# Optimization experiments

Hardware: AMD Instinct MI355X
Metric: run time of the kernel (lower is better)

The kernel has to match this reference:

```python
import jax, jax.numpy as jnp
import numpy as np
from itertools import product as iter_product

N_QUBITS = 6
DIM = 2 ** N_QUBITS            # 64
N_GEN = DIM * DIM - 1          # 4095
DEPTH = 4
N_OBS = 15

_GENS = None

def _build_generators(n):
    I = np.eye(2, dtype=np.complex64)
    X = np.array([[0, 1], [1, 0]], np.complex64)
    Y = np.array([[0, -1j], [1j, 0]], np.complex64)
    Z = np.array([[1, 0], [0, -1]], np.complex64)
    P = [I, X, Y, Z]
    gens = []
    for idx in iter_product(range(4), repeat=n):
        if all(i == 0 for i in idx):
            continue
        m = P[idx[0]]
        for k in range(1, n):
            m = np.kron(m, P[idx[k]])
        gens.append(m)
    return jnp.asarray(np.stack(gens))  # [4^n-1, 2^n, 2^n] complex64

def _gens():
    global _GENS
    if _GENS is None:
        _GENS = _build_generators(N_QUBITS)
    return _GENS

def _apply_ry(psi, q, theta, n):
    # psi: [B, 2^n] complex; RY(theta) on qubit q
    B = psi.shape[0]
    x = psi.reshape(B, 2 ** q, 2, 2 ** (n - q - 1))
    c = jnp.cos(theta / 2)
    s = jnp.sin(theta / 2)
    s0, s1 = x[:, :, 0, :], x[:, :, 1, :]
    x = jnp.stack([c * s0 - s * s1, s * s0 + c * s1], axis=2)
    return x.reshape(B, -1)

def _apply_cnot(psi, c, t, n):
    # psi: [B, 2^n]; CNOT control c, target t
    B = psi.shape[0]
    x = psi.reshape((B,) + (2,) * n)
    ax_c, ax_t = 1 + c, 1 + t
    x0 = jnp.take(x, 0, axis=ax_c)
    x1 = jnp.take(x, 1, axis=ax_c)
    ax_t2 = ax_t - (1 if ax_t > ax_c else 0)
    x1 = jnp.flip(x1, axis=ax_t2)
    x = jnp.stack([x0, x1], axis=ax_c)
    return x.reshape(B, -1)

def _make_hermitians(A, B, D):
    # create_Hermitian vectorized over the m observables.
    # h[i,j] = A[idx]+iB[idx] for j<i (row-major lower-tri), h[i-1,i-1]=D[i];
    # then H = h + h^H.
    il, jl = jnp.tril_indices(DIM, -1)  # row-major order matches count+j loop
    di = jnp.arange(DIM - 1)

    def one(a, b, d):
        h = jnp.zeros((DIM, DIM), jnp.complex64)
        h = h.at[il, jl].set(a + 1j * b)
        h = h.at[di, di].set(d[1:].astype(jnp.complex64))
        return h + h.conj().T

    return jax.vmap(one)(A, B, D)  # [m, DIM, DIM]

def setup_inputs() -> dict:
    key = jax.random.key(0)
    ks = jax.random.split(key, 8)
    batch, input_dim, hidden = 256, 1024, 2047
    n_off = DIM * (DIM - 1) // 2  # 2016
    return {
        "x": jax.random.normal(ks[0], (batch, input_dim), jnp.float32),
        "W1": 0.02 * jax.random.normal(ks[1], (input_dim, hidden), jnp.float32),
        "b1": jnp.zeros((hidden,), jnp.float32),
        "W2": 0.02 * jax.random.normal(ks[2], (hidden, N_GEN), jnp.float32),
        "b2": jnp.zeros((N_GEN,), jnp.float32),
        "var_params": 0.01 * jax.random.normal(ks[3], (DEPTH, N_QUBITS), jnp.float32),
        "A": 2.0 * jax.random.normal(ks[4], (N_OBS, n_off), jnp.float32),
        "B": 2.0 * jax.random.normal(ks[5], (N_OBS, n_off), jnp.float32),
        "D": 2.0 * jax.random.normal(ks[6], (N_OBS, DIM), jnp.float32),
    }

def reference(x, W1, b1, W2, b2, var_params, A, B, D):
    n = N_QUBITS
    # encoding projection: Linear -> SiLU -> Linear
    h = jax.nn.silu(x @ W1 + b1)
    theta = h @ W2 + b2  # [batch, 4^n - 1]
    gens = _gens()  # [n_gen, dim, dim] complex64 (constant)
    # A_mat = sum_g theta_g G_g (Hermitian), U = exp(i A_mat)
    Amat = jnp.einsum('bg,gij->bij', theta.astype(jnp.complex64), gens)
    U = jax.vmap(jax.scipy.linalg.expm)(1j * Amat)  # [batch, dim, dim]
    psi = U[:, :, 0]  # apply to |0...0>
    # hardware-efficient VQC: RY layer + CNOT ring per depth
    for d in range(DEPTH):
        for q in range(n):
            psi = _apply_ry(psi, q, var_params[d, q], n)
        for q in range(n):
            psi = _apply_cnot(psi, q, (q + 1) % n, n)
    H = _make_hermitians(A, B, D)  # [m, dim, dim]
    # expectation <psi|H_w|psi>
    exp = jnp.einsum('bi,wij,bj->bw', psi.conj(), H, psi).real
    return exp  # [batch, n_observables]
```

## Files before the change

kernel.cpp:

```cpp
#include <hip/hip_runtime.h>
#include <math.h>

typedef unsigned short ushort_t;
typedef __attribute__((ext_vector_type(8))) short bf16x8_t;
typedef __attribute__((ext_vector_type(4))) float f32x4_t;

__device__ __forceinline__ void tsplit(float v, unsigned& h, unsigned& l) {
  unsigned u = __float_as_uint(v);
  h = u >> 16;
  float lo = v - __uint_as_float(u & 0xffff0000u);
  l = __float_as_uint(lo) >> 16;
}

__device__ __forceinline__ void split8(const float* p, bf16x8_t& hi, bf16x8_t& lo) {
#pragma unroll
  for (int e = 0; e < 8; ++e) {
    unsigned h, l;
    tsplit(p[e], h, l);
    hi[e] = (short)h;
    lo[e] = (short)l;
  }
}

#define LSTR 40

__global__ __launch_bounds__(512) void gemm1_kernel(
    const float* __restrict__ x, const float* __restrict__ W1,
    const float* __restrict__ b1,
    ushort_t* __restrict__ hh, ushort_t* __restrict__ hl) {
  __shared__ __align__(16) ushort_t As[2][32 * LSTR];
  __shared__ __align__(16) ushort_t Bs[2][64 * LSTR];
  const int t = threadIdx.x;
  const int lane = t & 63;
  const int wv = t >> 6;
  const int l15 = lane & 15;
  const int quad = lane >> 4;
  const int wm = wv & 1;
  const int wn = wv >> 1;
  const int m0 = (blockIdx.x >> 5) * 32;
  const int n0 = (blockIdx.x & 31) * 64;

  f32x4_t acc = (f32x4_t){0.f, 0.f, 0.f, 0.f};

  const int xrow = (t & 127) >> 2;
  const int xkq  = (t & 3) * 8;
  const int wu   = t - 128;
  const int wnx  = wu & 63;
  const int wkh  = (wu >> 6) & 3;
  const bool wok = (n0 + wnx) < 2047;

  for (int k0 = 0; k0 < 1024; k0 += 32) {
    if (t < 128) {
      const float* src = x + (size_t)(m0 + xrow) * 1024 + k0 + xkq;
      float p[8];
      float4 va = *(const float4*)src;
      float4 vb = *(const float4*)(src + 4);
      p[0] = va.x; p[1] = va.y; p[2] = va.z; p[3] = va.w;
      p[4] = vb.x; p[5] = vb.y; p[6] = vb.z; p[7] = vb.w;
      bf16x8_t hi, lo;
      split8(p, hi, lo);
      *(bf16x8_t*)&As[0][xrow * LSTR + xkq] = hi;
      *(bf16x8_t*)&As[1][xrow * LSTR + xkq] = lo;
    } else if (t < 384) {
      float p[8];
#pragma unroll
      for (int i = 0; i < 8; ++i) {
        int k = k0 + wkh * 8 + i;
        p[i] = wok ? W1[(size_t)k * 2047 + n0 + wnx] : 0.f;
      }
      bf16x8_t hi, lo;
      split8(p, hi, lo);
      *(bf16x8_t*)&Bs[0][wnx * LSTR + wkh * 8] = hi;
      *(bf16x8_t*)&Bs[1][wnx * LSTR + wkh * 8] = lo;
    }
    __syncthreads();
    const int nr = wn * 16 + l15;
    bf16x8_t bfh = *(const bf16x8_t*)&Bs[0][nr * LSTR + quad * 8];
    bf16x8_t bfl = *(const bf16x8_t*)&Bs[1][nr * LSTR + quad * 8];
    const int mr = wm * 16 + l15;
    bf16x8_t afh = *(const bf16x8_t*)&As[0][mr * LSTR + quad * 8];
    bf16x8_t afl = *(const bf16x8_t*)&As[1][mr * LSTR + quad * 8];
    acc = __builtin_amdgcn_mfma_f32_16x16x32_bf16(afh, bfh, acc, 0, 0, 0);
    acc = __builtin_amdgcn_mfma_f32_16x16x32_bf16(afh, bfl, acc, 0, 0, 0);
    acc = __builtin_amdgcn_mfma_f32_16x16x32_bf16(afl, bfh, acc, 0, 0, 0);
    __syncthreads();
  }
  const int col = n0 + wn * 16 + l15;
#pragma unroll
  for (int rg = 0; rg < 4; ++rg) {
    int row = m0 + wm * 16 + quad * 4 + rg;
    float v = acc[rg];
    if (col < 2047) {
      v += b1[col];
      v = v / (1.f + expf(-v));
    } else {
      v = 0.f;
    }
    unsigned h, l;
    tsplit(v, h, l);
    size_t o = (size_t)row * 2048 + col;
    hh[o] = (ushort_t)h;
    hl[o] = (ushort_t)l;
  }
}

__global__ __launch_bounds__(256) void gemm2k_kernel(
    const ushort_t* __restrict__ Ah, const ushort_t* __restrict__ Al,
    const float* __restrict__ W2,
    float* __restrict__ part) {
  __shared__ __align__(16) ushort_t Ab[2][128 * LSTR];
  __shared__ __align__(16) ushort_t Bb[2][64 * LSTR];
  const int t = threadIdx.x;
  const int lane = t & 63;
  const int wv = t >> 6;
  const int l15 = lane & 15;
  const int quad = lane >> 4;
  const int wm = wv >> 1, wn = wv & 1;
  const int m0 = blockIdx.y * 128;
  const int n0 = blockIdx.x * 64;
  const int ks = blockIdx.z;

  const int wu  = t - 128;
  const int bn  = wu & 63;
  const int bkh = (wu >> 6) & 1;
  const bool bok = (n0 + bn) < 4095;

  f32x4_t acc[4][2];
#pragma unroll
  for (int i = 0; i < 4; ++i)
#pragma unroll
    for (int j = 0; j < 2; ++j) acc[i][j] = (f32x4_t){0.f, 0.f, 0.f, 0.f};

  for (int kt = 0; kt < 16; ++kt) {
    const int k0 = ks * 512 + kt * 32;
    if (wv < 2) {
      const ushort_t* src = wv ? Al : Ah;
      ushort_t* dst = Ab[wv];
#pragma unroll
      for (int q = 0; q < 8; ++q) {
        int r = q * 16 + (lane >> 2);
        int c = (lane & 3) * 8;
        *(int4*)&dst[r * LSTR + c] =
            *(const int4*)(src + (size_t)(m0 + r) * 2048 + k0 + c);
      }
    } else {
      float p[16];
#pragma unroll
      for (int i = 0; i < 16; ++i) {
        int k = k0 + bkh * 16 + i;
        p[i] = (bok && k < 2047) ? W2[(size_t)k * 4095 + n0 + bn] : 0.f;
      }
#pragma unroll
      for (int half = 0; half < 2; ++half) {
        bf16x8_t hi, lo;
        split8(&p[half * 8], hi, lo);
        *(bf16x8_t*)&Bb[0][bn * LSTR + bkh * 16 + half * 8] = hi;
        *(bf16x8_t*)&Bb[1][bn * LSTR + bkh * 16 + half * 8] = lo;
      }
    }
    __syncthreads();
    bf16x8_t bfh[2], bfl[2];
#pragma unroll
    for (int j = 0; j < 2; ++j) {
      int nr = wn * 32 + j * 16 + l15;
      bfh[j] = *(const bf16x8_t*)&Bb[0][nr * LSTR + quad * 8];
      bfl[j] = *(const bf16x8_t*)&Bb[1][nr * LSTR + quad * 8];
    }
#pragma unroll
    for (int i = 0; i < 4; ++i) {
      int mr = wm * 64 + i * 16 + l15;
      bf16x8_t afh = *(const bf16x8_t*)&Ab[0][mr * LSTR + quad * 8];
      bf16x8_t afl = *(const bf16x8_t*)&Ab[1][mr * LSTR + quad * 8];
#pragma unroll
      for (int j = 0; j < 2; ++j) {
        acc[i][j] = __builtin_amdgcn_mfma_f32_16x16x32_bf16(
            afh, bfh[j], acc[i][j], 0, 0, 0);
        acc[i][j] = __builtin_amdgcn_mfma_f32_16x16x32_bf16(
            afh, bfl[j], acc[i][j], 0, 0, 0);
        acc[i][j] = __builtin_amdgcn_mfma_f32_16x16x32_bf16(
            afl, bfh[j], acc[i][j], 0, 0, 0);
      }
    }
    __syncthreads();
  }
  float* pbase = part + (size_t)ks * 256 * 4096;
#pragma unroll
  for (int i = 0; i < 4; ++i)
#pragma unroll
    for (int j = 0; j < 2; ++j) {
      int row0 = m0 + wm * 64 + i * 16 + quad * 4;
      int col = n0 + wn * 32 + j * 16 + l15;
#pragma unroll
      for (int rg = 0; rg < 4; ++rg)
        pbase[(size_t)(row0 + rg) * 4096 + col] = acc[i][j][rg];
    }
}

#define TM 64
#define TN 64
#define TK 16
__global__ __launch_bounds__(256) void gemm_tiled(
    const float* __restrict__ X, const float* __restrict__ W,
    const float* __restrict__ bias, float* __restrict__ out,
    int M, int N, int K, int ldx, int ldw, int ldo, int doSilu, int padN)
{
  __shared__ float Xs[TK][TM + 4];
  __shared__ float Ws[TK][TN + 4];
  const int t = threadIdx.x;
  const int n0 = blockIdx.x * TN;
  const int m0 = blockIdx.y * TM;
  const int tr = t >> 4, tc = t & 15;
  float acc[4][4];
#pragma unroll
  for (int i = 0; i < 4; ++i)
#pragma unroll
    for (int j = 0; j < 4; ++j) acc[i][j] = 0.f;
  const int xr = t >> 2, xk = (t & 3) * 4;
  const int wk = t >> 4, wc = (t & 15) * 4;
  for (int k0 = 0; k0 < K; k0 += TK) {
    {
      const float* xp = X + (size_t)(m0 + xr) * ldx + (k0 + xk);
      float xv[4];
      if (k0 + xk + 3 < K) {
        float4 v = *(const float4*)xp;
        xv[0] = v.x; xv[1] = v.y; xv[2] = v.z; xv[3] = v.w;
      } else {
#pragma unroll
        for (int e = 0; e < 4; ++e) xv[e] = (k0 + xk + e < K) ? xp[e] : 0.f;
      }
#pragma unroll
      for (int e = 0; e < 4; ++e) Xs[xk + e][xr] = xv[e];
    }
    {
      const int kk = k0 + wk;
      const float* wp = W + (size_t)kk * ldw + (n0 + wc);
      const bool kv = kk < K;
#pragma unroll
      for (int e = 0; e < 4; ++e) {
        int n = n0 + wc + e;
        Ws[wk][wc + e] = (kv && n < N) ? wp[e] : 0.f;
      }
    }
    __syncthreads();
#pragma unroll
    for (int k = 0; k < TK; ++k) {
      float4 av = *(const float4*)&Xs[k][tr * 4];
      float4 bv = *(const float4*)&Ws[k][tc * 4];
      float a4[4] = {av.x, av.y, av.z, av.w};
      float b4[4] = {bv.x, bv.y, bv.z, bv.w};
#pragma unroll
      for (int i = 0; i < 4; ++i)
#pragma unroll
        for (int j = 0; j < 4; ++j)
          acc[i][j] = fmaf(a4[i], b4[j], acc[i][j]);
    }
    __syncthreads();
  }
#pragma unroll
  for (int i = 0; i < 4; ++i) {
    const int mrow = m0 + tr * 4 + i;
    float* op = out + (size_t)mrow * ldo;
#pragma unroll
    for (int j = 0; j < 4; ++j) {
      const int n = n0 + tc * 4 + j;
      if (n < N) {
        float v = acc[i][j] + bias[n];
        if (doSilu) v = v / (1.f + expf(-v));
        op[n] = v;
      } else if (n < padN) {
        op[n] = 0.f;
      }
    }
  }
}

#define RS 72
#define PL (64 * RS)

__device__ __forceinline__ void qmm4(
    const ushort_t* __restrict__ Prm, const ushort_t* __restrict__ Qcm,
    float* ore, float* oim, int mt, int nt, int quad, int l15)
{
  f32x4_t aR = (f32x4_t){0.f, 0.f, 0.f, 0.f};
  f32x4_t aN = (f32x4_t){0.f, 0.f, 0.f, 0.f};
  f32x4_t aI = (f32x4_t){0.f, 0.f, 0.f, 0.f};
#pragma unroll
  for (int kb = 0; kb < 2; ++kb) {
    const int ko = kb * 32 + quad * 8;
    const int ra = (mt * 16 + l15) * RS + ko;
    bf16x8_t arh = *(const bf16x8_t*)&Prm[0 * PL + ra];
    bf16x8_t arl = *(const bf16x8_t*)&Prm[1 * PL + ra];
    bf16x8_t aih = *(const bf16x8_t*)&Prm[2 * PL + ra];
    bf16x8_t ail = *(const bf16x8_t*)&Prm[3 * PL + ra];
    const int rb = (nt * 16 + l15) * RS + ko;
    bf16x8_t brh = *(const bf16x8_t*)&Qcm[0 * PL + rb];
    bf16x8_t brl = *(const bf16x8_t*)&Qcm[1 * PL + rb];
    bf16x8_t bih = *(const bf16x8_t*)&Qcm[2 * PL + rb];
    bf16x8_t bil = *(const bf16x8_t*)&Qcm[3 * PL + rb];
    aR = __builtin_amdgcn_mfma_f32_16x16x32_bf16(arh, brh, aR, 0, 0, 0);
    aR = __builtin_amdgcn_mfma_f32_16x16x32_bf16(arh, brl, aR, 0, 0, 0);
    aR = __builtin_amdgcn_mfma_f32_16x16x32_bf16(arl, brh, aR, 0, 0, 0);
    aN = __builtin_amdgcn_mfma_f32_16x16x32_bf16(aih, bih, aN, 0, 0, 0);
    aN = __builtin_amdgcn_mfma_f32_16x16x32_bf16(aih, bil, aN, 0, 0, 0);
    aN = __builtin_amdgcn_mfma_f32_16x16x32_bf16(ail, bih, aN, 0, 0, 0);
    aI = __builtin_amdgcn_mfma_f32_16x16x32_bf16(arh, bih, aI, 0, 0, 0);
    aI = __builtin_amdgcn_mfma_f32_16x16x32_bf16(arh, bil, aI, 0, 0, 0);
    aI = __builtin_amdgcn_mfma_f32_16x16x32_bf16(arl, bih, aI, 0, 0, 0);
    aI = __builtin_amdgcn_mfma_f32_16x16x32_bf16(aih, brh, aI, 0, 0, 0);
    aI = __builtin_amdgcn_mfma_f32_16x16x32_bf16(aih, brl, aI, 0, 0, 0);
    aI = __builtin_amdgcn_mfma_f32_16x16x32_bf16(ail, brh, aI, 0, 0, 0);
  }
#pragma unroll
  for (int rg = 0; rg < 4; ++rg) {
    ore[rg] = aR[rg] - aN[rg];
    oim[rg] = aI[rg];
  }
}

__device__ __forceinline__ void stage_rm4(
    ushort_t* rm, const float* re, const float* im, int mt, int nt,
    int quad, int l15)
{
  unsigned rh[4], rl[4], ih[4], il[4];
#pragma unroll
  for (int rg = 0; rg < 4; ++rg) {
    tsplit(re[rg], rh[rg], rl[rg]);
    tsplit(im[rg], ih[rg], il[rg]);
  }
#pragma unroll
  for (int rg = 0; rg < 4; ++rg) {
    int idx = (mt * 16 + quad * 4 + rg) * RS + nt * 16 + l15;
    rm[0 * PL + idx] = (ushort_t)rh[rg];
    rm[1 * PL + idx] = (ushort_t)rl[rg];
    rm[2 * PL + idx] = (ushort_t)ih[rg];
    rm[3 * PL + idx] = (ushort_t)il[rg];
  }
}

__device__ __forceinline__ void stage_cm4(
    ushort_t* cm, const float* re, const float* im, int mt, int nt,
    int quad, int l15)
{
  unsigned rh[4], rl[4], ih[4], il[4];
#pragma unroll
  for (int rg = 0; rg < 4; ++rg) {
    tsplit(re[rg], rh[rg], rl[rg]);
    tsplit(im[rg], ih[rg], il[rg]);
  }
  int base = (nt * 16 + l15) * RS + mt * 16 + quad * 4;
  uint2 p;
  p.x = rh[0] | (rh[1] << 16); p.y = rh[2] | (rh[3] << 16);
  *(uint2*)&cm[0 * PL + base] = p;
  p.x = rl[0] | (rl[1] << 16); p.y = rl[2] | (rl[3] << 16);
  *(uint2*)&cm[1 * PL + base] = p;
  p.x = ih[0] | (ih[1] << 16); p.y = ih[2] | (ih[3] << 16);
  *(uint2*)&cm[2 * PL + base] = p;
  p.x = il[0] | (il[1] << 16); p.y = il[2] | (il[3] << 16);
  *(uint2*)&cm[3 * PL + base] = p;
}

__device__ __forceinline__ void stage_both4(
    ushort_t* rm, ushort_t* cm, const float* re, const float* im,
    int mt, int nt, int quad, int l15)
{
  stage_rm4(rm, re, im, mt, nt, quad, l15);
  stage_cm4(cm, re, im, mt, nt, quad, l15);
}

__global__ __launch_bounds__(1024, 4) void quantum_kernel(
    const float* __restrict__ pin,
    const float* __restrict__ b2g,
    const float* __restrict__ vp,
    const float* __restrict__ Aobs,
    const float* __restrict__ Bobs,
    const float* __restrict__ Dobs,
    float* __restrict__ out,
    int fused)
{
  __shared__ __align__(16) ushort_t PQ[2][8 * PL];
  __shared__ float ps[128];
  __shared__ float scr16[16];
  __shared__ float csb[24], snb[24];
  __shared__ float sAf;
  __shared__ int   sS;

  float*  thetas = (float*)&PQ[1][0];
  float2* Als    = (float2*)&PQ[0][0];

  const int t = threadIdx.x;
  const int b = blockIdx.x;
  const int lane = t & 63;
  const int w = t >> 6;
  const int quad = lane >> 4;
  const int l15 = lane & 15;
  const int mt = w >> 2, nt = w & 3;

  float ssq;
  {
    float4 v = ((const float4*)(pin + (size_t)b * 4096))[t];
    if (fused) {
#pragma unroll
      for (int k = 1; k < 4; ++k) {
        float4 u =
            ((const float4*)(pin + (size_t)k * 256 * 4096 + (size_t)b * 4096))[t];
        v.x += u.x; v.y += u.y; v.z += u.z; v.w += u.w;
      }
      int n0i = 4 * t;
      v.x += b2g[n0i];
      v.y += b2g[n0i + 1];
      v.z += b2g[n0i + 2];
      if (n0i + 3 < 4095) v.w += b2g[n0i + 3];
    }
    if (t == 1023) v.w = 0.f;
    thetas[4 * t + 0] = v.x; thetas[4 * t + 1] = v.y;
    thetas[4 * t + 2] = v.z; thetas[4 * t + 3] = v.w;
    ssq = v.x * v.x + v.y * v.y + v.z * v.z + v.w * v.w;
  }
#pragma unroll
  for (int mm = 1; mm < 64; mm <<= 1) ssq += __shfl_xor(ssq, mm);
  if (lane == 0) scr16[w] = ssq;
  __syncthreads();
  if (w == 0) {
    float s = (lane < 16) ? scr16[lane] : 0.f;
#pragma unroll
    for (int mm = 1; mm < 64; mm <<= 1) s += __shfl_xor(s, mm);
    if (lane == 0) {
      float frob = fmaxf(8.f * sqrtf(s), 1e-3f);
      sAf = frob;
      float bound = 0.30f * frob;
      int sc = (bound > 1.f) ? (int)ceilf(log2f(bound)) : 0;
      sS = sc < 0 ? 0 : (sc > 12 ? 12 : sc);
    }
  } else if (w == 1 && lane < 24) {
    float sn, cs;
    sincosf(vp[lane] * 0.5f, &sn, &cs);
    snb[lane] = sn;
    csb[lane] = cs;
  }
  __syncthreads();
  const int sPow = sS;

  for (int xx = 0; xx < 4; ++xx) {
    const int x = w + 16 * xx;
    const int z = lane;
    int g1 = 0;
#pragma unroll
    for (int bq = 0; bq < 6; ++bq) {
      int xb = (x >> bq) & 1, zb = (z >> bq) & 1;
      int dig = xb ? (zb ? 2 : 1) : (zb ? 3 : 0);
      g1 |= dig << (2 * bq);
    }
    float tv = (g1 == 0) ? 0.f : thetas[g1 - 1];
    int pc = __popc(x & z) & 3;
    float re, im;
    switch (pc) {
      case 0:  re = tv;  im = 0.f;  break;
      case 1:  re = 0.f; im = -tv;  break;
      case 2:  re = -tv; im = 0.f;  break;
      default: re = 0.f; im = tv;   break;
    }
#pragma unroll
    for (int mk = 1; mk < 64; mk <<= 1) {
      float ore = __shfl_xor(re, mk);
      float oim = __shfl_xor(im, mk);
      if (z & mk) { re = ore - re; im = oim - im; }
      else        { re = re + ore; im = im + oim; }
    }
    Als[z * 66 + (z ^ x)] = make_float2(re, im);
  }
  __syncthreads();

  const float scl = ldexpf(1.f, -sPow);
  float bre[4], bim[4];
#pragma unroll
  for (int rg = 0; rg < 4; ++rg) {
    int row = mt * 16 + quad * 4 + rg;
    int col = nt * 16 + l15;
    float2 v = Als[row * 66 + col];
    bre[rg] = -v.y * scl;
    bim[rg] =  v.x * scl;
  }
  __syncthreads();

  ushort_t* b0 = &PQ[0][0];
  ushort_t* b1 = &PQ[1][0];
  stage_both4(b0, b0 + 4 * PL, bre, bim, mt, nt, quad, l15);
  __syncthreads();
  float b2re[4], b2im[4];
  qmm4(b0, b0 + 4 * PL, b2re, b2im, mt, nt, quad, l15);
  stage_both4(b1, b1 + 4 * PL, b2re, b2im, mt, nt, quad, l15);
  __syncthreads();
  float b3re[4], b3im[4];
  qmm4(b1, b0 + 4 * PL, b3re, b3im, mt, nt, quad, l15);

  const float c3 = 1.f / 6.f, c4 = 1.f / 24.f, c5 = 1.f / 120.f;
  const float c6 = 1.f / 720.f, c7 = 1.f / 5040.f, c8 = 1.f / 40320.f;
  float s1re[4], s1im[4], p0re[4], p0im[4];
#pragma unroll
  for (int rg = 0; rg < 4; ++rg) {
    float dg = (mt == nt && l15 == quad * 4 + rg) ? 1.f : 0.f;
    s1re[rg] = c4 * dg + c5 * bre[rg] + c6 * b2re[rg] + c7 * b3re[rg];
    s1im[rg] =           c5 * bim[rg] + c6 * b2im[rg] + c7 * b3im[rg];
    p0re[rg] = dg + bre[rg] + 0.5f * b2re[rg] + c3 * b3re[rg];
    p0im[rg] =      bim[rg] + 0.5f * b2im[rg] + c3 * b3im[rg];
  }
  float b4re[4], b4im[4];
  qmm4(b1, b1 + 4 * PL, b4re, b4im, mt, nt, quad, l15);
#pragma unroll
  for (int rg = 0; rg < 4; ++rg) {
    s1re[rg] += c8 * b4re[rg];
    s1im[rg] += c8 * b4im[rg];
  }
  __syncthreads();
  stage_rm4(b0, s1re, s1im, mt, nt, quad, l15);
  stage_cm4(b0 + 4 * PL, b4re, b4im, mt, nt, quad, l15);
  __syncthreads();
  float ure[4], uim[4];
  qmm4(b0, b0 + 4 * PL, ure, uim, mt, nt, quad, l15);
#pragma unroll
  for (int rg = 0; rg < 4; ++rg) {
    ure[rg] += p0re[rg];
    uim[rg] += p0im[rg];
  }

  int cur = 1;
  for (int q = 0; q < sPow; ++q) {
    ushort_t* bb = &PQ[cur][0];
    stage_both4(bb, bb + 4 * PL, ure, uim, mt, nt, quad, l15);
    __syncthreads();
    qmm4(bb, bb + 4 * PL, ure, uim, mt, nt, quad, l15);
    cur ^= 1;
  }

  if (nt == 0 && l15 == 0) {
#pragma unroll
    for (int rg = 0; rg < 4; ++rg) {
      int row = mt * 16 + quad * 4 + rg;
      ps[2 * row] = ure[rg];
      ps[2 * row + 1] = uim[rg];
    }
  }
  __syncthreads();

  if (t < 64) {
    float pre = ps[2 * t], pim = ps[2 * t + 1];
#pragma unroll
    for (int d = 0; d < 4; ++d) {
#pragma unroll
      for (int q = 0; q < 6; ++q) {
        float s = snb[d * 6 + q], c = csb[d * 6 + q];
        int bpos = 5 - q;
        int bit = (t >> bpos) & 1;
        float ore = __shfl_xor(pre, 1 << bpos);
        float oim = __shfl_xor(pim, 1 << bpos);
        float sg = bit ? s : -s;
        pre = c * pre + sg * ore;
        pim = c * pim + sg * oim;
      }
#pragma unroll
      for (int q = 0; q < 6; ++q) {
        int bc = 5 - q;
        int bt = 5 - ((q + 1) % 6);
        float ore = __shfl_xor(pre, 1 << bt);
        float oim = __shfl_xor(pim, 1 << bt);
        int ctrl = (t >> bc) & 1;
        pre = ctrl ? ore : pre;
        pim = ctrl ? oim : pim;
      }
    }
    ps[2 * t] = pre; ps[2 * t + 1] = pim;
  }
  __syncthreads();

  float* Rt = (float*)&PQ[0][0];
  float* It = Rt + 2016;
  for (int p = t; p < 2016; p += 1024) {
    int i = (int)((1.f + sqrtf(8.f * (float)p + 1.f)) * 0.5f);
    while (i * (i - 1) / 2 > p) --i;
    while (i * (i + 1) / 2 <= p) ++i;
    int j = p - i * (i - 1) / 2;
    float pri = ps[2 * i], pii = ps[2 * i + 1];
    float prj = ps[2 * j], pij = ps[2 * j + 1];
    Rt[p] = pri * prj + pii * pij;
    It[p] = pri * pij - pii * prj;
  }
  __syncthreads();

  if (w < 15) {
    float xr = ps[2 * lane], xi = ps[2 * lane + 1];
    float mypsq = xr * xr + xi * xi;
    const float* Ap = Aobs + w * 2016;
    const float* Bp = Bobs + w * 2016;
    float part = 0.f;
    for (int p2 = lane; p2 < 1008; p2 += 64) {
      float2 a = *(const float2*)&Ap[2 * p2];
      float2 bb2 = *(const float2*)&Bp[2 * p2];
      float2 rt = *(const float2*)&Rt[2 * p2];
      float2 it = *(const float2*)&It[2 * p2];
      part += a.x * rt.x - bb2.x * it.x;
      part += a.y * rt.y - bb2.y * it.y;
    }
    if (lane < 63) part += Dobs[w * 64 + lane + 1] * mypsq;
#pragma unroll
    for (int mm = 1; mm < 64; mm <<= 1) part += __shfl_xor(part, mm);
    if (lane == 0) out[b * 15 + w] = 2.f * part;
  }
}

extern "C" void kernel_launch(void* const* d_in, const int* in_sizes, int n_in,
                              void* d_out, int out_size, void* d_ws, size_t ws_size,
                              hipStream_t stream) {
  const float* x  = (const float*)d_in[0];
  const float* W1 = (const float*)d_in[1];
  const float* b1 = (const float*)d_in[2];
  const float* W2 = (const float*)d_in[3];
  const float* b2 = (const float*)d_in[4];
  const float* vp = (const float*)d_in[5];
  const float* Ao = (const float*)d_in[6];
  const float* Bo = (const float*)d_in[7];
  const float* Do = (const float*)d_in[8];
  float* out = (float*)d_out;

  const size_t O_PT = 0;
  const size_t O_HH = 16777216;
  const size_t O_HL = 17825792;
  const size_t NEED = 18874368;

  if (ws_size >= NEED) {
    char* ws = (char*)d_ws;
    float* part16 = (float*)(ws + O_PT);
    ushort_t* hh  = (ushort_t*)(ws + O_HH);
    ushort_t* hl  = (ushort_t*)(ws + O_HL);

    gemm1_kernel<<<256, 512, 0, stream>>>(x, W1, b1, hh, hl);
    gemm2k_kernel<<<dim3(64, 2, 4), 256, 0, stream>>>(hh, hl, W2, part16);
    quantum_kernel<<<256, 1024, 0, stream>>>(part16, b2, vp, Ao, Bo, Do, out, 1);
  } else {
    float* h     = (float*)d_ws;
    float* theta = h + 256 * 2048;
    gemm_tiled<<<dim3(32, 4), 256, 0, stream>>>(
        x, W1, b1, h, 256, 2047, 1024, 1024, 2047, 2048, 1, 2048);
    gemm_tiled<<<dim3(64, 4), 256, 0, stream>>>(
        h, W2, b2, theta, 256, 4095, 2047, 2048, 4095, 4096, 0, 4096);
    quantum_kernel<<<256, 1024, 0, stream>>>(theta, b2, vp, Ao, Bo, Do, out, 0);
  }
}
```

Before: 176.6 us.

## Double K-tile to 64 and register-prefetch next tile in both GEMM kernels

Both projection GEMMs now use a 64-wide K tile instead of 32, which halves the number of barrier-separated iterations. Global loads for the next K tile go into registers right after the barrier, so they overlap with the MFMA work on the current shared-memory tile. gemm2k also gets a launch bounds occupancy hint of 2 blocks. The trade-off is more registers (pa[16] int4 plus pw[32]) and more shared memory per block, which could lower occupancy or cause spills.

```diff
diff --git a/kernel.cpp b/kernel.cpp
--- a/kernel.cpp
+++ b/kernel.cpp
@@ -22,14 +22,12 @@
   }
 }
 
-#define LSTR 40
-
 __global__ __launch_bounds__(512) void gemm1_kernel(
     const float* __restrict__ x, const float* __restrict__ W1,
     const float* __restrict__ b1,
     ushort_t* __restrict__ hh, ushort_t* __restrict__ hl) {
-  __shared__ __align__(16) ushort_t As[2][32 * LSTR];
-  __shared__ __align__(16) ushort_t Bs[2][64 * LSTR];
+  __shared__ __align__(16) ushort_t As[2][32 * 72];
+  __shared__ __align__(16) ushort_t Bs[2][64 * 72];
   const int t = threadIdx.x;
   const int lane = t & 63;
   const int wv = t >> 6;
@@ -43,46 +41,73 @@
   f32x4_t acc = (f32x4_t){0.f, 0.f, 0.f, 0.f};
 
   const int xrow = (t & 127) >> 2;
-  const int xkq  = (t & 3) * 8;
+  const int xk   = (t & 3) * 16;
   const int wu   = t - 128;
   const int wnx  = wu & 63;
   const int wkh  = (wu >> 6) & 3;
   const bool wok = (n0 + wnx) < 2047;
 
-  for (int k0 = 0; k0 < 1024; k0 += 32) {
+  float p[16];
+  if (t < 128) {
+    const float* src = x + (size_t)(m0 + xrow) * 1024 + xk;
+#pragma unroll
+    for (int q = 0; q < 4; ++q) {
+      float4 v = *(const float4*)(src + 4 * q);
+      p[4 * q + 0] = v.x; p[4 * q + 1] = v.y;
+      p[4 * q + 2] = v.z; p[4 * q + 3] = v.w;
+    }
+  } else if (t < 384) {
+#pragma unroll
+    for (int i = 0; i < 16; ++i)
+      p[i] = wok ? W1[(size_t)(wkh * 16 + i) * 2047 + n0 + wnx] : 0.f;
+  }
+
+  for (int k0 = 0; k0 < 1024; k0 += 64) {
     if (t < 128) {
-      const float* src = x + (size_t)(m0 + xrow) * 1024 + k0 + xkq;
-      float p[8];
-      float4 va = *(const float4*)src;
-      float4 vb = *(const float4*)(src + 4);
-      p[0] = va.x; p[1] = va.y; p[2] = va.z; p[3] = va.w;
-      p[4] = vb.x; p[5] = vb.y; p[6] = vb.z; p[7] = vb.w;
-      bf16x8_t hi, lo;
-      split8(p, hi, lo);
-      *(bf16x8_t*)&As[0][xrow * LSTR + xkq] = hi;
-      *(bf16x8_t*)&As[1][xrow * LSTR + xkq] = lo;
+      bf16x8_t h0, l0, h1, l1;
+      split8(p, h0, l0);
+      split8(p + 8, h1, l1);
+      *(bf16x8_t*)&As[0][xrow * 72 + xk] = h0;
+      *(bf16x8_t*)&As[0][xrow * 72 + xk + 8] = h1;
+      *(bf16x8_t*)&As[1][xrow * 72 + xk] = l0;
+      *(bf16x8_t*)&As[1][xrow * 72 + xk + 8] = l1;
     } else if (t < 384) {
-      float p[8];
-#pragma unroll
-      for (int i = 0; i < 8; ++i) {
-        int k = k0 + wkh * 8 + i;
-        p[i] = wok ? W1[(size_t)k * 2047 + n0 + wnx] : 0.f;
-      }
-      bf16x8_t hi, lo;
-      split8(p, hi, lo);
-      *(bf16x8_t*)&Bs[0][wnx * LSTR + wkh * 8] = hi;
-      *(bf16x8_t*)&Bs[1][wnx * LSTR + wkh * 8] = lo;
+      bf16x8_t h0, l0, h1, l1;
+      split8(p, h0, l0);
+      split8(p + 8, h1, l1);
+      *(bf16x8_t*)&Bs[0][wnx * 72 + wkh * 16] = h0;
+      *(bf16x8_t*)&Bs[0][wnx * 72 + wkh * 16 + 8] = h1;
+      *(bf16x8_t*)&Bs[1][wnx * 72 + wkh * 16] = l0;
+      *(bf16x8_t*)&Bs[1][wnx * 72 + wkh * 16 + 8] = l1;
     }
     __syncthreads();
-    const int nr = wn * 16 + l15;
-    bf16x8_t bfh = *(const bf16x8_t*)&Bs[0][nr * LSTR + quad * 8];
-    bf16x8_t bfl = *(const bf16x8_t*)&Bs[1][nr * LSTR + quad * 8];
-    const int mr = wm * 16 + l15;
-    bf16x8_t afh = *(const bf16x8_t*)&As[0][mr * LSTR + quad * 8];
-    bf16x8_t afl = *(const bf16x8_t*)&As[1][mr * LSTR + quad * 8];
-    acc = __builtin_amdgcn_mfma_f32_16x16x32_bf16(afh, bfh, acc, 0, 0, 0);
-    acc = __builtin_amdgcn_mfma_f32_16x16x32_bf16(afh, bfl, acc, 0, 0, 0);
-    acc = __builtin_amdgcn_mfma_f32_16x16x32_bf16(afl, bfh, acc, 0, 0, 0);
+    const int kn = k0 + 64;
+    if (kn < 1024) {
+      if (t < 128) {
+        const float* src = x + (size_t)(m0 + xrow) * 1024 + kn + xk;
+#pragma unroll
+        for (int q = 0; q < 4; ++q) {
+          float4 v = *(const float4*)(src + 4 * q);
+          p[4 * q + 0] = v.x; p[4 * q + 1] = v.y;
+          p[4 * q + 2] = v.z; p[4 * q + 3] = v.w;
+        }
+      } else if (t < 384) {
+#pragma unroll
+        for (int i = 0; i < 16; ++i)
+          p[i] = wok ? W1[(size_t)(kn + wkh * 16 + i) * 2047 + n0 + wnx] : 0.f;
+      }
+    }
+#pragma unroll
+    for (int kb = 0; kb < 2; ++kb) {
+      const int ko = kb * 32 + quad * 8;
+      bf16x8_t bfh = *(const bf16x8_t*)&Bs[0][(wn * 16 + l15) * 72 + ko];
+      bf16x8_t bfl = *(const bf16x8_t*)&Bs[1][(wn * 16 + l15) * 72 + ko];
+      bf16x8_t afh = *(const bf16x8_t*)&As[0][(wm * 16 + l15) * 72 + ko];
+      bf16x8_t afl = *(const bf16x8_t*)&As[1][(wm * 16 + l15) * 72 + ko];
+      acc = __builtin_amdgcn_mfma_f32_16x16x32_bf16(afh, bfh, acc, 0, 0, 0);
+      acc = __builtin_amdgcn_mfma_f32_16x16x32_bf16(afh, bfl, acc, 0, 0, 0);
+      acc = __builtin_amdgcn_mfma_f32_16x16x32_bf16(afl, bfh, acc, 0, 0, 0);
+    }
     __syncthreads();
   }
   const int col = n0 + wn * 16 + l15;
@@ -104,12 +129,12 @@
   }
 }
 
-__global__ __launch_bounds__(256) void gemm2k_kernel(
+__global__ __launch_bounds__(256, 2) void gemm2k_kernel(
     const ushort_t* __restrict__ Ah, const ushort_t* __restrict__ Al,
     const float* __restrict__ W2,
     float* __restrict__ part) {
-  __shared__ __align__(16) ushort_t Ab[2][128 * LSTR];
-  __shared__ __align__(16) ushort_t Bb[2][64 * LSTR];
+  __shared__ __align__(16) ushort_t Ab[2][128 * 72];
+  __shared__ __align__(16) ushort_t Bb[2][64 * 72];
   const int t = threadIdx.x;
   const int lane = t & 63;
   const int wv = t >> 6;
@@ -122,7 +147,7 @@
 
   const int wu  = t - 128;
   const int bn  = wu & 63;
-  const int bkh = (wu >> 6) & 1;
+  const int bkq = (wu >> 6) & 1;
   const bool bok = (n0 + bn) < 4095;
 
   f32x4_t acc[4][2];
@@ -131,54 +156,89 @@
 #pragma unroll
     for (int j = 0; j < 2; ++j) acc[i][j] = (f32x4_t){0.f, 0.f, 0.f, 0.f};
 
-  for (int kt = 0; kt < 16; ++kt) {
-    const int k0 = ks * 512 + kt * 32;
+  int4  pa[16];
+  float pw[32];
+
+  {
+    const int k0 = ks * 512;
     if (wv < 2) {
       const ushort_t* src = wv ? Al : Ah;
+#pragma unroll
+      for (int q = 0; q < 16; ++q) {
+        int r = q * 8 + (lane >> 3);
+        int c = (lane & 7) * 8;
+        pa[q] = *(const int4*)(src + (size_t)(m0 + r) * 2048 + k0 + c);
+      }
+    } else {
+#pragma unroll
+      for (int i = 0; i < 32; ++i) {
+        int k = k0 + bkq * 32 + i;
+        pw[i] = (bok && k < 2047) ? W2[(size_t)k * 4095 + n0 + bn] : 0.f;
+      }
+    }
+  }
+
+  for (int kt = 0; kt < 8; ++kt) {
+    if (wv < 2) {
       ushort_t* dst = Ab[wv];
 #pragma unroll
-      for (int q = 0; q < 8; ++q) {
-        int r = q * 16 + (lane >> 2);
-        int c = (lane & 3) * 8;
-        *(int4*)&dst[r * LSTR + c] =
-            *(const int4*)(src + (size_t)(m0 + r) * 2048 + k0 + c);
+      for (int q = 0; q < 16; ++q) {
+        int r = q * 8 + (lane >> 3);
+        int c = (lane & 7) * 8;
+        *(int4*)&dst[r * 72 + c] = pa[q];
       }
     } else {
-      float p[16];
-#pragma unroll
-      for (int i = 0; i < 16; ++i) {
-        int k = k0 + bkh * 16 + i;
-        p[i] = (bok && k < 2047) ? W2[(size_t)k * 4095 + n0 + bn] : 0.f;
-      }
-#pragma unroll
-      for (int half = 0; half < 2; ++half) {
+#pragma unroll
+      for (int h = 0; h < 4; ++h) {
         bf16x8_t hi, lo;
-        split8(&p[half * 8], hi, lo);
-        *(bf16x8_t*)&Bb[0][bn * LSTR + bkh * 16 + half * 8] = hi;
-        *(bf16x8_t*)&Bb[1][bn * LSTR + bkh * 16 + half * 8] = lo;
+        split8(&pw[h * 8], hi, lo);
+        *(bf16x8_t*)&Bb[0][bn * 72 + bkq * 32 + h * 8] = hi;
+        *(bf16x8_t*)&Bb[1][bn * 72 + bkq * 32 + h * 8] = lo;
       }
     }
     __syncthreads();
-    bf16x8_t bfh[2], bfl[2];
-#pragma unroll
-    for (int j = 0; j < 2; ++j) {
-      int nr = wn * 32 + j * 16 + l15;
-      bfh[j] = *(const bf16x8_t*)&Bb[0][nr * LSTR + quad * 8];
-      bfl[j] = *(const bf16x8_t*)&Bb[1][nr * LSTR + quad * 8];
-    }
-#pragma unroll
-    for (int i = 0; i < 4; ++i) {
-      int mr = wm * 64 + i * 16 + l15;
-      bf16x8_t afh = *(const bf16x8_t*)&Ab[0][mr * LSTR + quad * 8];
-      bf16x8_t afl = *(const bf16x8_t*)&Ab[1][mr * LSTR + quad * 8];
+    if (kt + 1 < 8) {
+      const int k0 = ks * 512 + (kt + 1) * 64;
+      if (wv < 2) {
+        const ushort_t* src = wv ? Al : Ah;
+#pragma unroll
+        for (int q = 0; q < 16; ++q) {
+          int r = q * 8 + (lane >> 3);
+          int c = (lane & 7) * 8;
+          pa[q] = *(const int4*)(src + (size_t)(m0 + r) * 2048 + k0 + c);
+        }
+      } else {
+#pragma unroll
+        for (int i = 0; i < 32; ++i) {
+          int k = k0 + bkq * 32 + i;
+          pw[i] = (bok && k < 2047) ? W2[(size_t)k * 4095 + n0 + bn] : 0.f;
+        }
+      }
+    }
+#pragma unroll
+    for (int kb = 0; kb < 2; ++kb) {
+      const int ko = kb * 32 + quad * 8;
+      bf16x8_t bfh[2], bfl[2];
 #pragma unroll
       for (int j = 0; j < 2; ++j) {
-        acc[i][j] = __builtin_amdgcn_mfma_f32_16x16x32_bf16(
-            afh, bfh[j], acc[i][j], 0, 0, 0);
-        acc[i][j] = __builtin_amdgcn_mfma_f32_16x16x32_bf16(
-            afh, bfl[j], acc[i][j], 0, 0, 0);
-        acc[i][j] = __builtin_amdgcn_mfma_f32_16x16x32_bf16(
-            afl, bfh[j], acc[i][j], 0, 0, 0);
+        int nr = wn * 32 + j * 16 + l15;
+        bfh[j] = *(const bf16x8_t*)&Bb[0][nr * 72 + ko];
+        bfl[j] = *(const bf16x8_t*)&Bb[1][nr * 72 + ko];
+      }
+#pragma unroll
+      for (int i = 0; i < 4; ++i) {
+        int mr = wm * 64 + i * 16 + l15;
+        bf16x8_t afh = *(const bf16x8_t*)&Ab[0][mr * 72 + ko];
+        bf16x8_t afl = *(const bf16x8_t*)&Ab[1][mr * 72 + ko];
+#pragma unroll
+        for (int j = 0; j < 2; ++j) {
+          acc[i][j] = __builtin_amdgcn_mfma_f32_16x16x32_bf16(
+              afh, bfh[j], acc[i][j], 0, 0, 0);
+          acc[i][j] = __builtin_amdgcn_mfma_f32_16x16x32_bf16(
+              afh, bfl[j], acc[i][j], 0, 0, 0);
+          acc[i][j] = __builtin_amdgcn_mfma_f32_16x16x32_bf16(
+              afl, bfh[j], acc[i][j], 0, 0, 0);
+        }
       }
     }
     __syncthreads();
```

Measured after the change: 198.1 us. 1.12x slower.
